# Kernel optimization log

Hardware: AMD Instinct MI355X
Metric: run time of the kernel (lower is better)

The kernel has to match this reference:

```python
import jax, jax.numpy as jnp
import numpy as np

N, D, IN, HID, OUT, E = 20000, 8, 64, 128, 64, 100000
EPS = 1e-5


def _bn(h, g, b):
    # training-mode BatchNorm1d: biased batch variance, eps=1e-5
    m = h.mean(axis=0)
    v = jnp.mean((h - m) ** 2, axis=0)
    return (h - m) * jax.lax.rsqrt(v + EPS) * g + b


def setup_inputs() -> dict:
    key = jax.random.key(0)
    ks = jax.random.split(key, 12)
    x = jax.random.normal(ks[0], (N, IN), dtype=jnp.float32)
    node_ts = jax.random.uniform(ks[1], (N,), dtype=jnp.float32)
    neighbor_idx = jax.random.randint(ks[2], (N, D), 0, N, dtype=jnp.int32)
    neighbor_ts = jax.random.uniform(ks[3], (N, D), dtype=jnp.float32)
    target = jax.random.randint(ks[4], (2, E), 0, N, dtype=jnp.int32)
    neg_pairs = jax.random.randint(ks[5], (2, E), 0, N, dtype=jnp.int32)
    W1 = jax.random.normal(ks[6], (IN, HID), dtype=jnp.float32) * (1.0 / np.sqrt(IN))
    b1 = jnp.zeros((HID,), jnp.float32)
    g1 = jnp.ones((HID,), jnp.float32)
    be1 = jnp.zeros((HID,), jnp.float32)
    W2 = jax.random.normal(ks[7], (HID, OUT), dtype=jnp.float32) * (1.0 / np.sqrt(HID))
    b2 = jnp.zeros((OUT,), jnp.float32)
    g2 = jnp.ones((OUT,), jnp.float32)
    be2 = jnp.zeros((OUT,), jnp.float32)
    Wd = jax.random.normal(ks[8], (OUT, 1), dtype=jnp.float32) * (1.0 / np.sqrt(OUT))
    bd = jnp.zeros((1,), jnp.float32)
    return {"x": x, "node_ts": node_ts, "neighbor_idx": neighbor_idx,
            "neighbor_ts": neighbor_ts, "target": target, "neg_pairs": neg_pairs,
            "W1": W1, "b1": b1, "g1": g1, "be1": be1,
            "W2": W2, "b2": b2, "g2": g2, "be2": be2, "Wd": Wd, "bd": bd}


def reference(x, node_ts, neighbor_idx, neighbor_ts, target, neg_pairs,
              W1, b1, g1, be1, W2, b2, g2, be2, Wd, bd):
    n = jnp.arange(N, dtype=neighbor_idx.dtype)
    # ---- level-2 queries: every node at its own timestamp ----
    # children = D temporal-neighbor slots + self (self always valid, ts=node_ts)
    c_idx = jnp.concatenate([neighbor_idx, n[:, None]], axis=1)          # [N, D+1]
    c_ts = jnp.concatenate([neighbor_ts, node_ts[:, None]], axis=1)      # [N, D+1]
    mask2 = jnp.concatenate([neighbor_ts <= node_ts[:, None],
                             jnp.ones((N, 1), bool)], axis=1)            # [N, D+1]
    # ---- level-1 queries: each (child node, child ts) pair ----
    ci = c_idx.reshape(-1)                                               # [M]
    cts = c_ts.reshape(-1)
    gc_idx = jnp.concatenate([neighbor_idx[ci], ci[:, None]], axis=1)    # [M, D+1]
    mask1 = jnp.concatenate([neighbor_ts[ci] <= cts[:, None],
                             jnp.ones((ci.shape[0], 1), bool)], axis=1)
    # ---- layer 0: raw features of grandchildren ----
    h0 = x[gc_idx]                                                       # [M, D+1, IN]
    m1 = mask1.astype(x.dtype)
    agg1 = jnp.einsum('mk,mkf->mf', m1, h0) / m1.sum(1, keepdims=True)   # masked mean
    h1 = jax.nn.relu(_bn(agg1 @ W1 + b1, g1, be1))                       # [M, HID]
    h1 = h1.reshape(N, D + 1, HID)
    # ---- layer 2 aggregation over temporal children ----
    m2 = mask2.astype(x.dtype)
    agg2 = jnp.einsum('nk,nkf->nf', m2, h1) / m2.sum(1, keepdims=True)
    embs = jax.nn.relu(_bn(agg2 @ W2 + b2, g2, be2))                     # [N, OUT]
    # ---- HadNet link decoder + BCEWithLogits ----
    pos = (embs[target[0]] * embs[target[1]]) @ Wd + bd                  # [E, 1]
    neg = (embs[neg_pairs[0]] * embs[neg_pairs[1]]) @ Wd + bd            # [E, 1]
    preds = jnp.concatenate([pos, neg], axis=0)[:, 0]                    # [2E]
    labels = jnp.concatenate([jnp.ones((E,), x.dtype), jnp.zeros((E,), x.dtype)])
    loss = jnp.mean(jnp.maximum(preds, 0.0) - preds * labels
                    + jnp.log1p(jnp.exp(-jnp.abs(preds))))
    return loss
```

## Files before the change

kernel.cpp:

```cpp
#include <hip/hip_runtime.h>
#include <math.h>

constexpr int kN = 20000;
constexpr int kD = 8;
constexpr int kE = 100000;
constexpr int kM = kN * 9;
constexpr int kTiles1 = kM / 16;
constexpr int kTilesN = kN / 16;
constexpr float kEps = 1e-5f;

constexpr int S_SUM1 = 0, S_SQ1 = 128, S_SUM2 = 256, S_SQ2 = 320;

constexpr size_t OFF_M     = 0;
constexpr size_t OFF_PRE2  = 23040000;
constexpr size_t OFF_STATS = 25600000;
constexpr size_t OFF_CNT   = 25601536;
constexpr size_t OFF_RI    = 26321536;

typedef short short8 __attribute__((ext_vector_type(8)));
typedef float floatx4 __attribute__((ext_vector_type(4)));

__device__ __forceinline__ unsigned f2bf(float f) {
  unsigned u = __float_as_uint(f);
  u += 0x7fffu + ((u >> 16) & 1u);
  return u >> 16;
}

__global__ __launch_bounds__(256) void k0_prefix(
    const float* __restrict__ x, const float* __restrict__ node_ts,
    const int* __restrict__ nidx, const float* __restrict__ nts,
    unsigned short* __restrict__ M, int* __restrict__ rowinfo,
    float* __restrict__ cntf, float* __restrict__ out)
{
  if (blockIdx.x == 0 && threadIdx.x == 0) *out = 0.f;

  int c = blockIdx.x * 4 + (threadIdx.x >> 6);
  const int lane = threadIdx.x & 63;
  c = __builtin_amdgcn_readfirstlane(c);

  float4 t0 = *(const float4*)&nts[c * kD];
  float4 t1 = *(const float4*)&nts[c * kD + 4];
  int4   i0 = *(const int4*)&nidx[c * kD];
  int4   i1 = *(const int4*)&nidx[c * kD + 4];
  float ts[8] = {t0.x, t0.y, t0.z, t0.w, t1.x, t1.y, t1.z, t1.w};
  int   id[8] = {i0.x, i0.y, i0.z, i0.w, i1.x, i1.y, i1.z, i1.w};

#define CSWAP(A, B)                                                   \
  { float ta = ts[A], tb = ts[B]; int ia = id[A], ib = id[B];         \
    bool sw = tb < ta;                                                \
    ts[A] = sw ? tb : ta; ts[B] = sw ? ta : tb;                       \
    id[A] = sw ? ib : ia; id[B] = sw ? ia : ib; }
  CSWAP(0, 1) CSWAP(2, 3) CSWAP(0, 2) CSWAP(1, 3) CSWAP(1, 2)
  CSWAP(4, 5) CSWAP(6, 7) CSWAP(4, 6) CSWAP(5, 7) CSWAP(5, 6)
  CSWAP(0, 4) CSWAP(1, 5) CSWAP(2, 6) CSWAP(3, 7)
  CSWAP(2, 4) CSWAP(3, 5)
  CSWAP(1, 2) CSWAP(3, 4) CSWAP(5, 6)
#undef CSWAP

  float s = x[c * 64 + lane];
  unsigned short* mp = M + (size_t)c * 9 * 64 + lane;
  mp[0] = (unsigned short)f2bf(s);
#pragma unroll
  for (int r = 1; r <= kD; ++r) {
    s += x[id[r - 1] * 64 + lane];
    mp[r * 64] = (unsigned short)f2bf(s / (float)(r + 1));
  }

  const int m = blockIdx.x * 256 + threadIdx.x;
  if (m < kM) {
    const int n = (int)((unsigned)m / 9u);
    const int slot = m - n * 9;
    int cc; float t;
    if (slot < kD) { cc = nidx[n * kD + slot]; t = nts[n * kD + slot]; }
    else           { cc = n;                   t = node_ts[n]; }
    float4 a = *(const float4*)&nts[cc * kD];
    float4 b = *(const float4*)&nts[cc * kD + 4];
    int rank = (a.x <= t) + (a.y <= t) + (a.z <= t) + (a.w <= t)
             + (b.x <= t) + (b.y <= t) + (b.z <= t) + (b.w <= t);
    rowinfo[m] = cc * 9 + rank;
    atomicAdd(&cntf[cc * 9 + rank], 1.0f);
  }
}

__global__ __launch_bounds__(256, 3) void k1_stats(
    const unsigned short* __restrict__ M, const float* __restrict__ cntf,
    const float* __restrict__ W1, const float* __restrict__ b1,
    float* __restrict__ stats)
{
  __shared__ unsigned short W1T[128 * 72];
  __shared__ float redS[256][8];
  __shared__ float redQ[256][8];

  const int tid = threadIdx.x;
  const int lane = tid & 63;
  const int wave = tid >> 6;
  const int l15 = lane & 15;
  const int q = lane >> 4;

  for (int i = tid; i < 8192; i += 256) {
    int n = i >> 6, k = i & 63;
    W1T[n * 72 + k] = (unsigned short)f2bf(W1[k * 128 + n]);
  }
  __syncthreads();

  short8 bf[8][2];
#pragma unroll
  for (int cc = 0; cc < 8; ++cc)
#pragma unroll
    for (int s = 0; s < 2; ++s)
      bf[cc][s] = *(const short8*)&W1T[(cc * 16 + l15) * 72 + q * 8 + s * 32];

  float b1c[8];
#pragma unroll
  for (int cc = 0; cc < 8; ++cc) b1c[cc] = b1[cc * 16 + l15];

  float sum8[8], sq8[8];
#pragma unroll
  for (int cc = 0; cc < 8; ++cc) { sum8[cc] = 0.f; sq8[cc] = 0.f; }

  const int gw = blockIdx.x * 4 + wave;
  const int nw = gridDim.x * 4;

  for (int t = gw; t < kTiles1; t += nw) {
    const unsigned short* mp = M + (size_t)(t * 16 + l15) * 64;
    short8 af0 = *(const short8*)(mp + q * 8);
    short8 af1 = *(const short8*)(mp + 32 + q * 8);
    float c4[4];
#pragma unroll
    for (int i = 0; i < 4; ++i) c4[i] = cntf[t * 16 + q * 4 + i];

    floatx4 acc[8];
#pragma unroll
    for (int cc = 0; cc < 8; ++cc) {
      acc[cc] = (floatx4){0.f, 0.f, 0.f, 0.f};
      acc[cc] = __builtin_amdgcn_mfma_f32_16x16x32_bf16(af0, bf[cc][0], acc[cc], 0, 0, 0);
      acc[cc] = __builtin_amdgcn_mfma_f32_16x16x32_bf16(af1, bf[cc][1], acc[cc], 0, 0, 0);
    }
#pragma unroll
    for (int cc = 0; cc < 8; ++cc) {
#pragma unroll
      for (int i = 0; i < 4; ++i) {
        float v = acc[cc][i] + b1c[cc];
        sum8[cc] += c4[i] * v;
        sq8[cc]  += c4[i] * v * v;
      }
    }
  }

  __syncthreads();
#pragma unroll
  for (int cc = 0; cc < 8; ++cc) { redS[tid][cc] = sum8[cc]; redQ[tid][cc] = sq8[cc]; }
  __syncthreads();
  if (tid < 128) {
    int cc = tid >> 4, r15 = tid & 15;
    float s = 0.f, qq = 0.f;
#pragma unroll
    for (int w = 0; w < 4; ++w)
#pragma unroll
      for (int p = 0; p < 4; ++p) {
        int T = w * 64 + p * 16 + r15;
        s += redS[T][cc]; qq += redQ[T][cc];
      }
    atomicAdd(&stats[S_SUM1 + tid], s);
    atomicAdd(&stats[S_SQ1 + tid], qq);
  }
}

__global__ __launch_bounds__(256, 2) void k3_fused(
    const unsigned short* __restrict__ M, const int* __restrict__ rowinfo,
    const float* __restrict__ node_ts, const float* __restrict__ nts,
    const float* __restrict__ stats_in, const float* __restrict__ g1,
    const float* __restrict__ be1, const float* __restrict__ W1,
    const float* __restrict__ b1, const float* __restrict__ W2,
    const float* __restrict__ b2, float* __restrict__ stats_out,
    unsigned short* __restrict__ pre2)
{
  __shared__ __attribute__((aligned(16))) unsigned short W1T[128 * 72];
  __shared__ __attribute__((aligned(16))) unsigned short W2T[64 * 136];
  __shared__ __attribute__((aligned(16))) unsigned short sm[144 * 132];
  __shared__ __attribute__((aligned(16))) unsigned short aggT[16 * 136];
  __shared__ float wlds[144];
  __shared__ float winv[16];

  const int tid = threadIdx.x;
  const int lane = tid & 63;
  const int wave = tid >> 6;
  const int l15 = lane & 15;
  const int q = lane >> 4;

  int tb = blockIdx.x;
  int ri0 = rowinfo[tb * 144 + wave * 16 + l15];
  int ri1 = rowinfo[tb * 144 + 64 + wave * 16 + l15];
  int ri2 = 0;
  if (wave == 0) ri2 = rowinfo[tb * 144 + 128 + l15];

  for (int i = tid; i < 8192; i += 256) {
    int nn = i >> 6, k = i & 63;
    W1T[nn * 72 + k] = (unsigned short)f2bf(W1[k * 128 + nn]);
  }
  for (int i = tid; i < 8192; i += 256) {
    int nn = i >> 7, k = i & 127;
    W2T[nn * 136 + k] = (unsigned short)f2bf(W2[k * 64 + nn]);
  }
  __syncthreads();

  short8 bf[8][2];
  float scc[8], shc[8];
#pragma unroll
  for (int cc = 0; cc < 8; ++cc) {
    int col = cc * 16 + l15;
#pragma unroll
    for (int s = 0; s < 2; ++s)
      bf[cc][s] = *(const short8*)&W1T[col * 72 + q * 8 + s * 32];
    float mean = stats_in[S_SUM1 + col] * (1.f / kM);
    float var  = stats_in[S_SQ1 + col] * (1.f / kM) - mean * mean;
    float sg   = g1[col] * rsqrtf(var + kEps);
    scc[cc] = sg;
    shc[cc] = (b1[col] - mean) * sg + be1[col];
  }
  short8 bfr2[4];
#pragma unroll
  for (int s = 0; s < 4; ++s)
    bfr2[s] = *(const short8*)&W2T[(wave * 16 + l15) * 136 + q * 8 + s * 32];
  const float b2w = b2[wave * 16 + l15];

  float sumS = 0.f, sumQ = 0.f;

  for (; tb < kTilesN; tb += gridDim.x) {
    const int node0 = tb * 16;

    const unsigned short* mp0 = M + (size_t)ri0 * 64;
    const unsigned short* mp1 = M + (size_t)ri1 * 64;
    short8 a00 = *(const short8*)(mp0 + q * 8);
    short8 a01 = *(const short8*)(mp0 + 32 + q * 8);
    short8 a10 = *(const short8*)(mp1 + q * 8);
    short8 a11 = *(const short8*)(mp1 + 32 + q * 8);
    short8 a20{}, a21{};
    if (wave == 0) {
      const unsigned short* mp2 = M + (size_t)ri2 * 64;
      a20 = *(const short8*)(mp2 + q * 8);
      a21 = *(const short8*)(mp2 + 32 + q * 8);
    }

    {
      int ntb = tb + gridDim.x;
      if (ntb < kTilesN) {
        ri0 = rowinfo[ntb * 144 + wave * 16 + l15];
        ri1 = rowinfo[ntb * 144 + 64 + wave * 16 + l15];
        if (wave == 0) ri2 = rowinfo[ntb * 144 + 128 + l15];
      }
    }

    if (tid < 144) {
      int ln = tid / 9;
      int slot = tid - ln * 9;
      int nn = node0 + ln;
      float w = 1.f;
      if (slot < kD) w = (nts[nn * kD + slot] <= node_ts[nn]) ? 1.f : 0.f;
      wlds[tid] = w;
    }
    __syncthreads();
    if (tid < 16) {
      float swv = 0.f;
#pragma unroll
      for (int r = 0; r < 9; ++r) swv += wlds[tid * 9 + r];
      winv[tid] = 1.f / swv;
    }

#define ROWTILE(TL, A0, A1)                                                  \
    {                                                                        \
      floatx4 acc[8];                                                        \
      _Pragma("unroll")                                                      \
      for (int cc = 0; cc < 8; ++cc) {                                       \
        acc[cc] = (floatx4){0.f, 0.f, 0.f, 0.f};                             \
        acc[cc] = __builtin_amdgcn_mfma_f32_16x16x32_bf16(A0, bf[cc][0], acc[cc], 0, 0, 0); \
        acc[cc] = __builtin_amdgcn_mfma_f32_16x16x32_bf16(A1, bf[cc][1], acc[cc], 0, 0, 0); \
      }                                                                      \
      float w4[4];                                                           \
      _Pragma("unroll")                                                      \
      for (int i = 0; i < 4; ++i) w4[i] = wlds[(TL) * 16 + q * 4 + i];       \
      _Pragma("unroll")                                                      \
      for (int cc = 0; cc < 8; ++cc) {                                       \
        int col = cc * 16 + l15;                                             \
        _Pragma("unroll")                                                    \
        for (int i = 0; i < 4; ++i) {                                        \
          float val = fmaxf(fmaf(acc[cc][i], scc[cc], shc[cc]), 0.f) * w4[i];\
          sm[((TL) * 16 + q * 4 + i) * 132 + col] = (unsigned short)f2bf(val);\
        }                                                                    \
      }                                                                      \
    }
    ROWTILE(wave, a00, a01)
    ROWTILE(wave + 4, a10, a11)
    if (wave == 0) ROWTILE(8, a20, a21)
#undef ROWTILE
    __syncthreads();

#pragma unroll
    for (int k = 0; k < 4; ++k) {
      int it = tid + k * 256;
      int nd = it >> 6, cp = it & 63;
      float s0 = 0.f, s1 = 0.f;
#pragma unroll
      for (int r = 0; r < 9; ++r) {
        unsigned u = *(const unsigned*)&sm[(nd * 9 + r) * 132 + cp * 2];
        s0 += __uint_as_float(u << 16);
        s1 += __uint_as_float(u & 0xffff0000u);
      }
      float iv = winv[nd];
      *(unsigned*)&aggT[nd * 136 + cp * 2] = f2bf(s0 * iv) | (f2bf(s1 * iv) << 16);
    }
    __syncthreads();

    short8 af2[4];
#pragma unroll
    for (int s = 0; s < 4; ++s)
      af2[s] = *(const short8*)&aggT[l15 * 136 + q * 8 + s * 32];
    floatx4 acc2 = (floatx4){0.f, 0.f, 0.f, 0.f};
#pragma unroll
    for (int s = 0; s < 4; ++s)
      acc2 = __builtin_amdgcn_mfma_f32_16x16x32_bf16(af2[s], bfr2[s], acc2, 0, 0, 0);
#pragma unroll
    for (int i = 0; i < 4; ++i) {
      float v = acc2[i] + b2w;
      int nrow = node0 + q * 4 + i;
      pre2[(size_t)nrow * 64 + wave * 16 + l15] = (unsigned short)f2bf(v);
      sumS += v; sumQ += v * v;
    }
  }

  sumS += __shfl_xor(sumS, 16); sumS += __shfl_xor(sumS, 32);
  sumQ += __shfl_xor(sumQ, 16); sumQ += __shfl_xor(sumQ, 32);
  if (lane < 16) {
    atomicAdd(&stats_out[S_SUM2 + wave * 16 + lane], sumS);
    atomicAdd(&stats_out[S_SQ2 + wave * 16 + lane], sumQ);
  }
}

__global__ __launch_bounds__(256) void k6_loss(
    const unsigned short* __restrict__ pre2, const float* __restrict__ stats,
    const float* __restrict__ g2, const float* __restrict__ be2,
    const float* __restrict__ Wd, const int* __restrict__ tgt,
    const int* __restrict__ neg, const float* __restrict__ bd,
    float* __restrict__ out)
{
  __shared__ float scl[64], shl[64], wdl[64];
  __shared__ float redl[256];
  const int tid = threadIdx.x;
  if (tid < 64) {
    float mean = stats[S_SUM2 + tid] * (1.f / kN);
    float var  = stats[S_SQ2 + tid] * (1.f / kN) - mean * mean;
    float s    = g2[tid] * rsqrtf(var + kEps);
    scl[tid] = s; shl[tid] = be2[tid] - mean * s; wdl[tid] = Wd[tid];
  }
  __syncthreads();

  const int tq = tid & 15;
  const int qb = tid >> 4;
  const int c0 = tq * 4;
  const float4 sc4 = {scl[c0], scl[c0 + 1], scl[c0 + 2], scl[c0 + 3]};
  const float4 sh4 = {shl[c0], shl[c0 + 1], shl[c0 + 2], shl[c0 + 3]};
  const float4 wd4 = {wdl[c0], wdl[c0 + 1], wdl[c0 + 2], wdl[c0 + 3]};
  const float bd0 = bd[0];

  float lsum = 0.f;
  const int e0 = blockIdx.x * 128 + qb * 8;
#pragma unroll
  for (int it = 0; it < 8; ++it) {
    int e = e0 + it;
    if (e < 2 * kE) {
      int i, j; float lab;
      if (e < kE) { i = tgt[e];      j = tgt[kE + e]; lab = 1.f; }
      else        { i = neg[e - kE]; j = neg[e];      lab = 0.f; }
      uint2 ua = *(const uint2*)&pre2[(size_t)i * 64 + c0];
      uint2 ub = *(const uint2*)&pre2[(size_t)j * 64 + c0];
      float a0 = __uint_as_float(ua.x << 16), a1 = __uint_as_float(ua.x & 0xffff0000u);
      float a2 = __uint_as_float(ua.y << 16), a3 = __uint_as_float(ua.y & 0xffff0000u);
      float b0 = __uint_as_float(ub.x << 16), b1v = __uint_as_float(ub.x & 0xffff0000u);
      float b2v = __uint_as_float(ub.y << 16), b3 = __uint_as_float(ub.y & 0xffff0000u);
      float ei0 = fmaxf(fmaf(a0, sc4.x, sh4.x), 0.f) * wd4.x;
      float ei1 = fmaxf(fmaf(a1, sc4.y, sh4.y), 0.f) * wd4.y;
      float ei2 = fmaxf(fmaf(a2, sc4.z, sh4.z), 0.f) * wd4.z;
      float ei3 = fmaxf(fmaf(a3, sc4.w, sh4.w), 0.f) * wd4.w;
      float ej0 = fmaxf(fmaf(b0, sc4.x, sh4.x), 0.f);
      float ej1 = fmaxf(fmaf(b1v, sc4.y, sh4.y), 0.f);
      float ej2 = fmaxf(fmaf(b2v, sc4.z, sh4.z), 0.f);
      float ej3 = fmaxf(fmaf(b3, sc4.w, sh4.w), 0.f);
      float p = ei0 * ej0 + ei1 * ej1 + ei2 * ej2 + ei3 * ej3;
      p += __shfl_xor(p, 1); p += __shfl_xor(p, 2);
      p += __shfl_xor(p, 4); p += __shfl_xor(p, 8);
      p += bd0;
      float l = fmaxf(p, 0.f) - p * lab + log1pf(expf(-fabsf(p)));
      if (tq == 0) lsum += l;
    }
  }
  redl[tid] = lsum;
  __syncthreads();
  for (int s = 128; s > 0; s >>= 1) {
    if (tid < s) redl[tid] += redl[tid + s];
    __syncthreads();
  }
  if (tid == 0) atomicAdd(out, redl[0] * (1.f / (2 * kE)));
}

extern "C" void kernel_launch(void* const* d_in, const int* in_sizes, int n_in,
                              void* d_out, int out_size, void* d_ws, size_t ws_size,
                              hipStream_t stream) {
  (void)in_sizes; (void)n_in; (void)out_size; (void)ws_size;
  const float* x       = (const float*)d_in[0];
  const float* node_ts = (const float*)d_in[1];
  const int*   nidx    = (const int*)d_in[2];
  const float* nts     = (const float*)d_in[3];
  const int*   tgt     = (const int*)d_in[4];
  const int*   neg     = (const int*)d_in[5];
  const float* W1      = (const float*)d_in[6];
  const float* b1      = (const float*)d_in[7];
  const float* g1      = (const float*)d_in[8];
  const float* be1     = (const float*)d_in[9];
  const float* W2      = (const float*)d_in[10];
  const float* b2      = (const float*)d_in[11];
  const float* g2      = (const float*)d_in[12];
  const float* be2     = (const float*)d_in[13];
  const float* Wd      = (const float*)d_in[14];
  const float* bd      = (const float*)d_in[15];

  char* ws = (char*)d_ws;
  unsigned short* Mbuf = (unsigned short*)(ws + OFF_M);
  unsigned short* pre2 = (unsigned short*)(ws + OFF_PRE2);
  float* stats = (float*)(ws + OFF_STATS);
  float* cntf  = (float*)(ws + OFF_CNT);
  int*   rinfo = (int*)(ws + OFF_RI);
  float* out   = (float*)d_out;

  hipMemsetAsync(ws + OFF_STATS, 0, 1536 + 720000, stream);

  k0_prefix<<<kN / 4, 256, 0, stream>>>(x, node_ts, nidx, nts, Mbuf, rinfo,
                                        cntf, out);
  k1_stats<<<704, 256, 0, stream>>>(Mbuf, cntf, W1, b1, stats);
  k3_fused<<<512, 256, 0, stream>>>(Mbuf, rinfo, node_ts, nts, stats, g1, be1,
                                    W1, b1, W2, b2, stats, pre2);
  k6_loss<<<(2 * kE + 127) / 128, 256, 0, stream>>>(pre2, stats, g2, be2, Wd,
                                                    tgt, neg, bd, out);
}
```

Baseline: 199.6 us.

## Prefetch next tile's gathered rows across loop iterations and use lgkm-only barriers

Moves the gather of the next tile's M rows (and the following tile's row indices) to just after the first MFMA stage, so those global loads are in flight during the LDS reduction and second GEMM. It also replaces __syncthreads with a barrier that waits only on LDS counters, so outstanding global prefetch loads do not stall the barriers. This keeps more registers live across the loop body and relies on the custom barrier being sufficient for the LDS dependencies.

```diff
diff --git a/kernel.cpp b/kernel.cpp
--- a/kernel.cpp
+++ b/kernel.cpp
@@ -24,6 +24,11 @@
   unsigned u = __float_as_uint(f);
   u += 0x7fffu + ((u >> 16) & 1u);
   return u >> 16;
+}
+
+__device__ __forceinline__ void lds_barrier() {
+  asm volatile("s_waitcnt lgkmcnt(0)" ::: "memory");
+  __builtin_amdgcn_s_barrier();
 }
 
 __global__ __launch_bounds__(256) void k0_prefix(
@@ -224,32 +229,32 @@
     bfr2[s] = *(const short8*)&W2T[(wave * 16 + l15) * 136 + q * 8 + s * 32];
   const float b2w = b2[wave * 16 + l15];
 
-  float sumS = 0.f, sumQ = 0.f;
-
-  for (; tb < kTilesN; tb += gridDim.x) {
-    const int node0 = tb * 16;
-
+  short8 a00, a01, a10, a11;
+  short8 a20 = short8{}, a21 = short8{};
+  {
     const unsigned short* mp0 = M + (size_t)ri0 * 64;
     const unsigned short* mp1 = M + (size_t)ri1 * 64;
-    short8 a00 = *(const short8*)(mp0 + q * 8);
-    short8 a01 = *(const short8*)(mp0 + 32 + q * 8);
-    short8 a10 = *(const short8*)(mp1 + q * 8);
-    short8 a11 = *(const short8*)(mp1 + 32 + q * 8);
-    short8 a20{}, a21{};
+    a00 = *(const short8*)(mp0 + q * 8);
+    a01 = *(const short8*)(mp0 + 32 + q * 8);
+    a10 = *(const short8*)(mp1 + q * 8);
+    a11 = *(const short8*)(mp1 + 32 + q * 8);
     if (wave == 0) {
       const unsigned short* mp2 = M + (size_t)ri2 * 64;
       a20 = *(const short8*)(mp2 + q * 8);
       a21 = *(const short8*)(mp2 + 32 + q * 8);
     }
-
-    {
-      int ntb = tb + gridDim.x;
-      if (ntb < kTilesN) {
-        ri0 = rowinfo[ntb * 144 + wave * 16 + l15];
-        ri1 = rowinfo[ntb * 144 + 64 + wave * 16 + l15];
-        if (wave == 0) ri2 = rowinfo[ntb * 144 + 128 + l15];
-      }
-    }
+  }
+  if (tb + (int)gridDim.x < kTilesN) {
+    int ntb = tb + gridDim.x;
+    ri0 = rowinfo[ntb * 144 + wave * 16 + l15];
+    ri1 = rowinfo[ntb * 144 + 64 + wave * 16 + l15];
+    if (wave == 0) ri2 = rowinfo[ntb * 144 + 128 + l15];
+  }
+
+  float sumS = 0.f, sumQ = 0.f;
+
+  for (; tb < kTilesN; tb += gridDim.x) {
+    const int node0 = tb * 16;
 
     if (tid < 144) {
       int ln = tid / 9;
@@ -259,7 +264,7 @@
       if (slot < kD) w = (nts[nn * kD + slot] <= node_ts[nn]) ? 1.f : 0.f;
       wlds[tid] = w;
     }
-    __syncthreads();
+    lds_barrier();
     if (tid < 16) {
       float swv = 0.f;
 #pragma unroll
@@ -293,7 +298,28 @@
     ROWTILE(wave + 4, a10, a11)
     if (wave == 0) ROWTILE(8, a20, a21)
 #undef ROWTILE
-    __syncthreads();
+
+    if (tb + (int)gridDim.x < kTilesN) {
+      const unsigned short* mp0 = M + (size_t)ri0 * 64;
+      const unsigned short* mp1 = M + (size_t)ri1 * 64;
+      a00 = *(const short8*)(mp0 + q * 8);
+      a01 = *(const short8*)(mp0 + 32 + q * 8);
+      a10 = *(const short8*)(mp1 + q * 8);
+      a11 = *(const short8*)(mp1 + 32 + q * 8);
+      if (wave == 0) {
+        const unsigned short* mp2 = M + (size_t)ri2 * 64;
+        a20 = *(const short8*)(mp2 + q * 8);
+        a21 = *(const short8*)(mp2 + 32 + q * 8);
+      }
+      int nntb = tb + 2 * gridDim.x;
+      if (nntb < kTilesN) {
+        ri0 = rowinfo[nntb * 144 + wave * 16 + l15];
+        ri1 = rowinfo[nntb * 144 + 64 + wave * 16 + l15];
+        if (wave == 0) ri2 = rowinfo[nntb * 144 + 128 + l15];
+      }
+    }
+
+    lds_barrier();
 
 #pragma unroll
     for (int k = 0; k < 4; ++k) {
@@ -309,7 +335,7 @@
       float iv = winv[nd];
       *(unsigned*)&aggT[nd * 136 + cp * 2] = f2bf(s0 * iv) | (f2bf(s1 * iv) << 16);
     }
-    __syncthreads();
+    lds_barrier();
 
     short8 af2[4];
 #pragma unroll
```

After: 199.7 us. Within noise of the previous version (+0.0%).
